# Kernel tuning notes

Hardware: AMD Instinct MI355X
Metric: run time of the kernel (lower is better)

Reference implementation:

```python
import jax, jax.numpy as jnp
import numpy as np

N = 100000
D = 256
E = 3200000


def setup_inputs() -> dict:
    key = jax.random.key(0)
    ks = jax.random.split(key, 8)
    x = jax.random.normal(ks[0], (N, D), dtype=jnp.float32)
    edge_index = jax.random.randint(ks[1], (2, E), 0, N, dtype=jnp.int64)
    s = 1.0 / np.sqrt(D)
    W_l = jax.random.uniform(ks[2], (D, D), dtype=jnp.float32, minval=-s, maxval=s)
    b_l = jax.random.uniform(ks[3], (D,), dtype=jnp.float32, minval=-s, maxval=s)
    W_r = jax.random.uniform(ks[4], (D, D), dtype=jnp.float32, minval=-s, maxval=s)
    ln_gamma = jnp.ones((D,), dtype=jnp.float32)
    ln_beta = jnp.zeros((D,), dtype=jnp.float32)
    return {"x": x, "edge_index": edge_index, "W_l": W_l, "b_l": b_l,
            "W_r": W_r, "ln_gamma": ln_gamma, "ln_beta": ln_beta}


def reference(x, edge_index, W_l, b_l, W_r, ln_gamma, ln_beta):
    src, dst = edge_index[0], edge_index[1]
    n = x.shape[0]
    # mean aggregation of neighbor (source) features onto destination nodes
    msg_sum = jax.ops.segment_sum(x[src], dst, num_segments=n)        # [N, D]
    deg = jax.ops.segment_sum(jnp.ones((src.shape[0],), x.dtype), dst,
                              num_segments=n)                          # [N]
    agg = msg_sum / jnp.maximum(deg, 1.0)[:, None]
    # SAGEConv: lin_l(agg) + lin_r(x)   (bias in lin_l only)
    f = agg @ W_l.T + b_l + x @ W_r.T
    # exact-erf GELU (torch F.gelu default)
    f = jax.nn.gelu(f, approximate=False)
    # LayerNorm over feature dim
    mu = jnp.mean(f, axis=-1, keepdims=True)
    var = jnp.var(f, axis=-1, keepdims=True)
    f = (f - mu) * jax.lax.rsqrt(var + 1e-5) * ln_gamma + ln_beta
    # dropout in eval mode = identity; residual add
    return f + x
```

## Files before the change

### kernel.cpp

```cpp
#include <hip/hip_runtime.h>

#define D 256
#define KDIM 512
#define BCAP 16384
#define EPB 8192
#define BM 128
#define BK 32
#define NT 16

typedef __bf16 bf16_t;
typedef bf16_t bf16x8 __attribute__((ext_vector_type(8)));
typedef bf16_t bf16x4 __attribute__((ext_vector_type(4)));
typedef float f32x4_t __attribute__((ext_vector_type(4)));
typedef float f32x2_t __attribute__((ext_vector_type(2)));

__device__ __forceinline__ void async_cp16(const void* g, void* l) {
    __builtin_amdgcn_global_load_lds(
        (const __attribute__((address_space(1))) unsigned int*)g,
        (__attribute__((address_space(3))) unsigned int*)l, 16, 0, 0);
}


__global__ __launch_bounds__(256) void k_scatter1(const int* __restrict__ eidx,
                                                  int* __restrict__ bcur,
                                                  int* __restrict__ staging, int E) {
    __shared__ int lhist[512];
    __shared__ int lcur[512];
    __shared__ int gbase[512];
    const int t = threadIdx.x;
    const int e0 = blockIdx.x * EPB;
    int e1 = e0 + EPB;
    if (e1 > E) e1 = E;

    lhist[t] = 0;
    lhist[t + 256] = 0;
    lcur[t] = 0;
    lcur[t + 256] = 0;
    __syncthreads();

    for (int e = e0 + t; e < e1; e += 256) {
        int d = eidx[E + e];
        atomicAdd(&lhist[d >> 8], 1);
    }
    __syncthreads();

#pragma unroll
    for (int b = t; b < 512; b += 256) {
        int c = lhist[b];
        gbase[b] = (c > 0) ? atomicAdd(&bcur[b * 16], c) : 0;
    }
    __syncthreads();

    for (int e = e0 + t; e < e1; e += 256) {
        int s = eidx[e];
        int d = eidx[E + e];
        int b = d >> 8;
        int pos = gbase[b] + atomicAdd(&lcur[b], 1);
        staging[(size_t)b * BCAP + pos] = ((d & 255) << 24) | s;
    }
}

__global__ __launch_bounds__(512) void k_bbase(const int* __restrict__ bcur,
                                               int* __restrict__ bbase,
                                               int* __restrict__ row_ptr,
                                               int B1, int N, int E) {
    __shared__ int sm[512];
    int t = threadIdx.x;
    int v = (t < B1) ? bcur[t * 16] : 0;
    sm[t] = v;
    __syncthreads();
    for (int off = 1; off < 512; off <<= 1) {
        int u = (t >= off) ? sm[t - off] : 0;
        __syncthreads();
        sm[t] += u;
        __syncthreads();
    }
    if (t < B1) bbase[t] = sm[t] - v;
    if (t == 0) row_ptr[N] = E;
}

__global__ __launch_bounds__(256) void k_bucket(const int* __restrict__ bcur,
                                                const int* __restrict__ bbase,
                                                const int* __restrict__ staging,
                                                int* __restrict__ edge_src,
                                                int* __restrict__ row_ptr, int N) {
    __shared__ int lhist[256];
    __shared__ int lscan[256];
    __shared__ int lcur[256];
    int b = blockIdx.x, t = threadIdx.x;
    int node_base = b << 8;
    int nn = N - node_base;
    if (nn > 256) nn = 256;
    int cnt = bcur[b * 16];
    int base = bbase[b];
    const int* stg = staging + (size_t)b * BCAP;

    lhist[t] = 0;
    __syncthreads();
    for (int i = t; i < cnt; i += 256)
        atomicAdd(&lhist[((unsigned)stg[i]) >> 24], 1);
    __syncthreads();
    int v = lhist[t];
    lscan[t] = v;
    __syncthreads();
    for (int off = 1; off < 256; off <<= 1) {
        int u = (t >= off) ? lscan[t - off] : 0;
        __syncthreads();
        lscan[t] += u;
        __syncthreads();
    }
    int excl = lscan[t] - v;
    if (t < nn) row_ptr[node_base + t] = base + excl;
    lscan[t] = excl;
    lcur[t] = 0;
    __syncthreads();
    for (int i = t; i < cnt; i += 256) {
        int w = stg[i];
        int ln = ((unsigned)w) >> 24;
        int src = w & 0xFFFFFF;
        int pos = base + lscan[ln] + atomicAdd(&lcur[ln], 1);
        edge_src[pos] = src;
    }
}


__global__ __launch_bounds__(256) void k_convx(const float* __restrict__ x,
                                               unsigned int* __restrict__ Xq,
                                               int total8) {
    int i = blockIdx.x * 256 + threadIdx.x;
    if (i >= total8) return;
    float4 v0 = *(const float4*)(x + (size_t)i * 8);
    float4 v1 = *(const float4*)(x + (size_t)i * 8 + 4);
    int w0 = 0, w1 = 0;
    w0 = __builtin_amdgcn_cvt_pk_fp8_f32(v0.x, v0.y, w0, false);
    w0 = __builtin_amdgcn_cvt_pk_fp8_f32(v0.z, v0.w, w0, true);
    w1 = __builtin_amdgcn_cvt_pk_fp8_f32(v1.x, v1.y, w1, false);
    w1 = __builtin_amdgcn_cvt_pk_fp8_f32(v1.z, v1.w, w1, true);
    uint2 o = {(unsigned)w0, (unsigned)w1};
    *(uint2*)(Xq + (size_t)i * 2) = o;
}

__global__ __launch_bounds__(256) void k_convw(const float* __restrict__ Wl,
                                               const float* __restrict__ Wr,
                                               bf16_t* __restrict__ Wcat) {
    int i = blockIdx.x * 256 + threadIdx.x;
    if (i >= D * KDIM / 4) return;
    int o = i * 4;
    int j = o >> 9;
    int k = o & 511;
    const float* src = (k < D) ? (Wl + (size_t)j * D + k)
                               : (Wr + (size_t)j * D + (k - D));
    float4 v = *(const float4*)src;
    bf16x4 ov = {(bf16_t)v.x, (bf16_t)v.y, (bf16_t)v.z, (bf16_t)v.w};
    *(bf16x4*)(Wcat + o) = ov;
}


__global__ __launch_bounds__(256) void k_aggregate(const int* __restrict__ row_ptr,
                                                   const int* __restrict__ edge_src,
                                                   const unsigned int* __restrict__ Xq,
                                                   bf16_t* __restrict__ Agg, int N) {
    int wv = threadIdx.x >> 6;
    int lane = threadIdx.x & 63;
    int node = blockIdx.x * 4 + wv;
    if (node >= N) return;
    int g = lane >> 4;
    int c = lane & 15;
    int beg = row_ptr[node];
    int end = row_ptr[node + 1];

    float acc[16];
#pragma unroll
    for (int k = 0; k < 16; k++) acc[k] = 0.f;

#define ACC4(w, bidx)                                            \
    {                                                            \
        f32x2_t lo = __builtin_amdgcn_cvt_pk_f32_fp8((w), false);\
        f32x2_t hi = __builtin_amdgcn_cvt_pk_f32_fp8((w), true); \
        acc[(bidx) + 0] += lo[0];                                \
        acc[(bidx) + 1] += lo[1];                                \
        acc[(bidx) + 2] += hi[0];                                \
        acc[(bidx) + 3] += hi[1];                                \
    }

    for (int j = beg; j < end; j += 8) {
        int j0 = j + g, j1 = j + 4 + g;
        bool ok0 = j0 < end, ok1 = j1 < end;
        int s0 = edge_src[ok0 ? j0 : beg];
        int s1 = edge_src[ok1 ? j1 : beg];
        uint4 v0 = *(const uint4*)(Xq + (size_t)s0 * 64 + c * 4);
        uint4 v1 = *(const uint4*)(Xq + (size_t)s1 * 64 + c * 4);
        if (!ok0) { v0.x = 0; v0.y = 0; v0.z = 0; v0.w = 0; }
        if (!ok1) { v1.x = 0; v1.y = 0; v1.z = 0; v1.w = 0; }
        ACC4(v0.x, 0) ACC4(v0.y, 4) ACC4(v0.z, 8) ACC4(v0.w, 12)
        ACC4(v1.x, 0) ACC4(v1.y, 4) ACC4(v1.z, 8) ACC4(v1.w, 12)
    }
#undef ACC4

#pragma unroll
    for (int k = 0; k < 16; k++) {
        acc[k] += __shfl_xor(acc[k], 16, 64);
        acc[k] += __shfl_xor(acc[k], 32, 64);
    }
    int dg = end - beg;
    float inv = 1.0f / (float)(dg > 0 ? dg : 1);
    if (g == 0) {
        bf16x8 o0 = {(bf16_t)(acc[0] * inv), (bf16_t)(acc[1] * inv),
                     (bf16_t)(acc[2] * inv), (bf16_t)(acc[3] * inv),
                     (bf16_t)(acc[4] * inv), (bf16_t)(acc[5] * inv),
                     (bf16_t)(acc[6] * inv), (bf16_t)(acc[7] * inv)};
        bf16x8 o1 = {(bf16_t)(acc[8] * inv), (bf16_t)(acc[9] * inv),
                     (bf16_t)(acc[10] * inv), (bf16_t)(acc[11] * inv),
                     (bf16_t)(acc[12] * inv), (bf16_t)(acc[13] * inv),
                     (bf16_t)(acc[14] * inv), (bf16_t)(acc[15] * inv)};
        *(bf16x8*)(Agg + (size_t)node * D + c * 16) = o0;
        *(bf16x8*)(Agg + (size_t)node * D + c * 16 + 8) = o1;
    }
}


__global__ __launch_bounds__(512) void k_gemm(const bf16_t* __restrict__ Agg,
                                              const bf16_t* __restrict__ Wcat,
                                              const float* __restrict__ x,
                                              const float* __restrict__ b_l,
                                              const float* __restrict__ gamma,
                                              const float* __restrict__ beta,
                                              float* __restrict__ out, int M) {
    __shared__ __align__(16) bf16_t As[2][BM * BK];
    __shared__ __align__(16) bf16_t Bs[2][D * BK];
    __shared__ float sm_s[4][BM];
    __shared__ float sm_q[4][BM];

    const int tid = threadIdx.x;
    const int lane = tid & 63;
    const int wid = tid >> 6;
    const int lr = lane & 15;
    const int lh = lane >> 4;
    const int wm = wid >> 2;
    const int wn = wid & 3;
    const int row0 = blockIdx.x * BM;

    const int sr = tid >> 2;
    const int sj = tid & 3;
    const int fA = (sr ^ (sr >> 2)) & 3;
    const int ar = (row0 + sr > M - 1) ? (M - 1) : (row0 + sr);
    const bf16_t* aggsrc = Agg + (size_t)ar * D + ((sj ^ fA) << 3);
    const float* xsrc = x + (size_t)ar * D + sj * 8;
    const int awr = sr * BK + ((sj ^ fA) << 3);
    const int rb1 = 128 + sr;
    const int fB1 = (rb1 ^ (rb1 >> 2)) & 3;
    const bf16_t* wsrc0 = Wcat + (size_t)sr * KDIM + ((sj ^ fA) << 3);
    const bf16_t* wsrc1 = Wcat + (size_t)rb1 * KDIM + ((sj ^ fB1) << 3);
    const int wbase8 = (tid & ~63) << 3;

#define STAGE(buf, k0)                                                         \
    do {                                                                       \
        async_cp16(wsrc0 + (k0), &Bs[buf][wbase8]);                            \
        async_cp16(wsrc1 + (k0), &Bs[buf][4096 + wbase8]);                     \
        if ((k0) < D) {                                                        \
            async_cp16(aggsrc + (k0), &As[buf][wbase8]);                       \
        } else {                                                               \
            float4 u0 = *(const float4*)(xsrc + (k0) - D);                     \
            float4 u1 = *(const float4*)(xsrc + (k0) - D + 4);                 \
            bf16x8 v = {(bf16_t)u0.x, (bf16_t)u0.y, (bf16_t)u0.z,              \
                        (bf16_t)u0.w, (bf16_t)u1.x, (bf16_t)u1.y,              \
                        (bf16_t)u1.z, (bf16_t)u1.w};                           \
            *(bf16x8*)&As[buf][awr] = v;                                       \
        }                                                                      \
    } while (0)

    f32x4_t acc[4][4];
#pragma unroll
    for (int i = 0; i < 4; i++)
#pragma unroll
        for (int j = 0; j < 4; j++) acc[i][j] = (f32x4_t){0.f, 0.f, 0.f, 0.f};

    STAGE(0, 0);
    __syncthreads();

#pragma unroll
    for (int t = 0; t < NT; ++t) {
        const int cur = t & 1;
        if (t + 1 < NT) STAGE(cur ^ 1, (t + 1) * BK);

        bf16x8 a[4], b[4];
#pragma unroll
        for (int mt = 0; mt < 4; mt++) {
            int ra = wm * 64 + mt * 16 + lr;
            int blk = lh ^ ((ra ^ (ra >> 2)) & 3);
            a[mt] = *(const bf16x8*)&As[cur][ra * BK + (blk << 3)];
        }
#pragma unroll
        for (int nt = 0; nt < 4; nt++) {
            int rbn = wn * 64 + nt * 16 + lr;
            int blk = lh ^ ((rbn ^ (rbn >> 2)) & 3);
            b[nt] = *(const bf16x8*)&Bs[cur][rbn * BK + (blk << 3)];
        }
#pragma unroll
        for (int mt = 0; mt < 4; mt++)
#pragma unroll
            for (int nt = 0; nt < 4; nt++)
                acc[mt][nt] = __builtin_amdgcn_mfma_f32_16x16x32_bf16(
                    a[mt], b[nt], acc[mt][nt], 0, 0, 0);
        __syncthreads();
    }
#undef STAGE

    float bl[4], ga[4], be[4];
#pragma unroll
    for (int nt = 0; nt < 4; nt++) {
        int c = wn * 64 + nt * 16 + lr;
        bl[nt] = b_l[c];
        ga[nt] = gamma[c];
        be[nt] = beta[c];
    }

#pragma unroll
    for (int mt = 0; mt < 4; mt++) {
#pragma unroll
        for (int r = 0; r < 4; r++) {
            float s = 0.f, q = 0.f;
#pragma unroll
            for (int nt = 0; nt < 4; nt++) {
                float u = acc[mt][nt][r] + bl[nt];
                float ge = 0.5f * u * (1.0f + erff(u * 0.70710678118654752f));
                acc[mt][nt][r] = ge;
                s += ge;
                q += ge * ge;
            }
#pragma unroll
            for (int off = 8; off >= 1; off >>= 1) {
                s += __shfl_xor(s, off, 64);
                q += __shfl_xor(q, off, 64);
            }
            if (lr == 0) {
                int rl = wm * 64 + mt * 16 + lh * 4 + r;
                sm_s[wn][rl] = s;
                sm_q[wn][rl] = q;
            }
        }
    }
    __syncthreads();

#pragma unroll
    for (int mt = 0; mt < 4; mt++) {
#pragma unroll
        for (int r = 0; r < 4; r++) {
            int rl = wm * 64 + mt * 16 + lh * 4 + r;
            int m = row0 + rl;
            float S = sm_s[0][rl] + sm_s[1][rl] + sm_s[2][rl] + sm_s[3][rl];
            float Q = sm_q[0][rl] + sm_q[1][rl] + sm_q[2][rl] + sm_q[3][rl];
            float mean = S * (1.0f / 256.0f);
            float var = Q * (1.0f / 256.0f) - mean * mean;
            float rstd = rsqrtf(var + 1e-5f);
            if (m < M) {
#pragma unroll
                for (int nt = 0; nt < 4; nt++) {
                    int c = wn * 64 + nt * 16 + lr;
                    out[(size_t)m * D + c] =
                        (acc[mt][nt][r] - mean) * rstd * ga[nt] + be[nt] +
                        x[(size_t)m * D + c];
                }
            }
        }
    }
}


extern "C" void kernel_launch(void* const* d_in, const int* in_sizes, int n_in,
                              void* d_out, int out_size, void* d_ws, size_t ws_size,
                              hipStream_t stream) {
    const float* x = (const float*)d_in[0];
    const int* eidx = (const int*)d_in[1];
    const float* W_l = (const float*)d_in[2];
    const float* b_l = (const float*)d_in[3];
    const float* W_r = (const float*)d_in[4];
    const float* gamma = (const float*)d_in[5];
    const float* beta = (const float*)d_in[6];
    float* out = (float*)d_out;

    const int N = in_sizes[0] / D;
    const int E = in_sizes[1] / 2;
    const int B1 = (N + 255) >> 8;

    char* basep = (char*)d_ws;
    size_t off = 0;
    auto take = [&](size_t bytes) -> void* {
        void* r = basep + off;
        off += (bytes + 255) & ~(size_t)255;
        return r;
    };
    bf16_t* Agg = (bf16_t*)take((size_t)N * D * sizeof(bf16_t));
    unsigned int* Xq = (unsigned int*)take((size_t)N * (D / 4) * 4);
    int* edge_src = (int*)take((size_t)E * sizeof(int));
    bf16_t* Wcat = (bf16_t*)take((size_t)D * KDIM * sizeof(bf16_t));
    int* row_ptr = (int*)take((size_t)(N + 1) * sizeof(int));
    int* bcur = (int*)take((size_t)B1 * 16 * sizeof(int));
    int* bbase = (int*)take((size_t)B1 * sizeof(int));
    int* staging = (int*)Agg;

    hipMemsetAsync(bcur, 0, (size_t)B1 * 16 * sizeof(int), stream);

    k_scatter1<<<(E + EPB - 1) / EPB, 256, 0, stream>>>(eidx, bcur, staging, E);
    k_bbase<<<1, 512, 0, stream>>>(bcur, bbase, row_ptr, B1, N, E);
    k_bucket<<<B1, 256, 0, stream>>>(bcur, bbase, staging, edge_src, row_ptr, N);

    k_convx<<<(N * (D / 8) + 255) / 256, 256, 0, stream>>>(x, Xq, N * (D / 8));
    k_convw<<<(D * KDIM / 4 + 255) / 256, 256, 0, stream>>>(W_l, W_r, Wcat);

    k_aggregate<<<(N + 3) / 4, 256, 0, stream>>>(row_ptr, edge_src, Xq, Agg, N);

    k_gemm<<<(N + BM - 1) / BM, 512, 0, stream>>>(Agg, Wcat, x, b_l, gamma,
                                                  beta, out, N);
}
```

Before: 325.9 us.

## Pre-convert x to bf16 and triple-buffer GEMM with async loads

The conversion kernel now also writes a bf16 copy of x, so the GEMM's x@W_r half can stage A tiles with async global-to-LDS copies instead of synchronous fp32 loads, conversion and LDS stores. The GEMM moves from a double buffer to a three-deep LDS ring with prefetch distance two. It uses explicit vmcnt waits plus one barrier per iteration instead of two __syncthreads. This costs an extra N×D bf16 buffer written in k_convx and more LDS per block, which may lower occupancy.

```diff
diff --git a/kernel.cpp b/kernel.cpp
--- a/kernel.cpp
+++ b/kernel.cpp
@@ -7,6 +7,7 @@
 #define BM 128
 #define BK 32
 #define NT 16
+#define DEPTH 3
 
 typedef __bf16 bf16_t;
 typedef bf16_t bf16x8 __attribute__((ext_vector_type(8)));
@@ -126,6 +127,7 @@
 
 __global__ __launch_bounds__(256) void k_convx(const float* __restrict__ x,
                                                unsigned int* __restrict__ Xq,
+                                               bf16_t* __restrict__ Xb,
                                                int total8) {
     int i = blockIdx.x * 256 + threadIdx.x;
     if (i >= total8) return;
@@ -138,6 +140,9 @@
     w1 = __builtin_amdgcn_cvt_pk_fp8_f32(v1.z, v1.w, w1, true);
     uint2 o = {(unsigned)w0, (unsigned)w1};
     *(uint2*)(Xq + (size_t)i * 2) = o;
+    bf16x8 ob = {(bf16_t)v0.x, (bf16_t)v0.y, (bf16_t)v0.z, (bf16_t)v0.w,
+                 (bf16_t)v1.x, (bf16_t)v1.y, (bf16_t)v1.z, (bf16_t)v1.w};
+    *(bf16x8*)(Xb + (size_t)i * 8) = ob;
 }
 
 __global__ __launch_bounds__(256) void k_convw(const float* __restrict__ Wl,
@@ -220,14 +225,15 @@
 
 
 __global__ __launch_bounds__(512) void k_gemm(const bf16_t* __restrict__ Agg,
+                                              const bf16_t* __restrict__ Xb,
                                               const bf16_t* __restrict__ Wcat,
                                               const float* __restrict__ x,
                                               const float* __restrict__ b_l,
                                               const float* __restrict__ gamma,
                                               const float* __restrict__ beta,
                                               float* __restrict__ out, int M) {
-    __shared__ __align__(16) bf16_t As[2][BM * BK];
-    __shared__ __align__(16) bf16_t Bs[2][D * BK];
+    __shared__ __align__(16) bf16_t As[DEPTH][BM * BK];
+    __shared__ __align__(16) bf16_t Bs[DEPTH][D * BK];
     __shared__ float sm_s[4][BM];
     __shared__ float sm_q[4][BM];
 
@@ -245,8 +251,7 @@
     const int fA = (sr ^ (sr >> 2)) & 3;
     const int ar = (row0 + sr > M - 1) ? (M - 1) : (row0 + sr);
     const bf16_t* aggsrc = Agg + (size_t)ar * D + ((sj ^ fA) << 3);
-    const float* xsrc = x + (size_t)ar * D + sj * 8;
-    const int awr = sr * BK + ((sj ^ fA) << 3);
+    const bf16_t* xbsrc = Xb + (size_t)ar * D + ((sj ^ fA) << 3);
     const int rb1 = 128 + sr;
     const int fB1 = (rb1 ^ (rb1 >> 2)) & 3;
     const bf16_t* wsrc0 = Wcat + (size_t)sr * KDIM + ((sj ^ fA) << 3);
@@ -255,18 +260,10 @@
 
 #define STAGE(buf, k0)                                                         \
     do {                                                                       \
+        async_cp16(((k0) < D) ? (aggsrc + (k0)) : (xbsrc + (k0) - D),          \
+                   &As[buf][wbase8]);                                          \
         async_cp16(wsrc0 + (k0), &Bs[buf][wbase8]);                            \
         async_cp16(wsrc1 + (k0), &Bs[buf][4096 + wbase8]);                     \
-        if ((k0) < D) {                                                        \
-            async_cp16(aggsrc + (k0), &As[buf][wbase8]);                       \
-        } else {                                                               \
-            float4 u0 = *(const float4*)(xsrc + (k0) - D);                     \
-            float4 u1 = *(const float4*)(xsrc + (k0) - D + 4);                 \
-            bf16x8 v = {(bf16_t)u0.x, (bf16_t)u0.y, (bf16_t)u0.z,              \
-                        (bf16_t)u0.w, (bf16_t)u1.x, (bf16_t)u1.y,              \
-                        (bf16_t)u1.z, (bf16_t)u1.w};                           \
-            *(bf16x8*)&As[buf][awr] = v;                                       \
-        }                                                                      \
     } while (0)
 
     f32x4_t acc[4][4];
@@ -276,13 +273,20 @@
         for (int j = 0; j < 4; j++) acc[i][j] = (f32x4_t){0.f, 0.f, 0.f, 0.f};
 
     STAGE(0, 0);
-    __syncthreads();
+    STAGE(1, BK);
 
 #pragma unroll
     for (int t = 0; t < NT; ++t) {
-        const int cur = t & 1;
-        if (t + 1 < NT) STAGE(cur ^ 1, (t + 1) * BK);
-
+        if (t < NT - 1) {
+            asm volatile("s_waitcnt vmcnt(3)" ::: "memory");
+        } else {
+            asm volatile("s_waitcnt vmcnt(0)" ::: "memory");
+        }
+        __builtin_amdgcn_s_barrier();
+        __builtin_amdgcn_sched_barrier(0);
+        if (t + 2 < NT) STAGE((t + 2) % DEPTH, (t + 2) * BK);
+
+        const int cur = t % DEPTH;
         bf16x8 a[4], b[4];
 #pragma unroll
         for (int mt = 0; mt < 4; mt++) {
@@ -302,7 +306,6 @@
             for (int nt = 0; nt < 4; nt++)
                 acc[mt][nt] = __builtin_amdgcn_mfma_f32_16x16x32_bf16(
                     a[mt], b[nt], acc[mt][nt], 0, 0, 0);
-        __syncthreads();
     }
 #undef STAGE
 
@@ -391,6 +394,7 @@
         return r;
     };
     bf16_t* Agg = (bf16_t*)take((size_t)N * D * sizeof(bf16_t));
+    bf16_t* Xb = (bf16_t*)take((size_t)N * D * sizeof(bf16_t));
     unsigned int* Xq = (unsigned int*)take((size_t)N * (D / 4) * 4);
     int* edge_src = (int*)take((size_t)E * sizeof(int));
     bf16_t* Wcat = (bf16_t*)take((size_t)D * KDIM * sizeof(bf16_t));
@@ -405,11 +409,11 @@
     k_bbase<<<1, 512, 0, stream>>>(bcur, bbase, row_ptr, B1, N, E);
     k_bucket<<<B1, 256, 0, stream>>>(bcur, bbase, staging, edge_src, row_ptr, N);
 
-    k_convx<<<(N * (D / 8) + 255) / 256, 256, 0, stream>>>(x, Xq, N * (D / 8));
+    k_convx<<<(N * (D / 8) + 255) / 256, 256, 0, stream>>>(x, Xq, Xb, N * (D / 8));
     k_convw<<<(D * KDIM / 4 + 255) / 256, 256, 0, stream>>>(W_l, W_r, Wcat);
 
     k_aggregate<<<(N + 3) / 4, 256, 0, stream>>>(row_ptr, edge_src, Xq, Agg, N);
 
-    k_gemm<<<(N + BM - 1) / BM, 512, 0, stream>>>(Agg, Wcat, x, b_l, gamma,
+    k_gemm<<<(N + BM - 1) / BM, 512, 0, stream>>>(Agg, Xb, Wcat, x, b_l, gamma,
                                                   beta, out, N);
 }
```

Result: slower. 337.9 us (+3.7%).
